# Optimization experiments

Hardware: AMD Instinct MI355X
Metric: run time of the kernel (lower is better)

Reference implementation:

```python
import jax, jax.numpy as jnp
import numpy as np

H = 64  # hidden size

def _uniform(key, shape, k):
    return jax.random.uniform(key, shape, jnp.float32, -k, k)

def setup_inputs() -> dict:
    key = jax.random.key(0)
    ks = jax.random.split(key, 20)
    k = 1.0 / np.sqrt(H)
    inp = {"x": jax.random.normal(ks[0], (4096, 512, 4), jnp.float32)}
    in_sizes = [4, H, H]
    for l in range(3):
        inp[f"w_ih{l}"] = _uniform(ks[1 + 4 * l], (H, in_sizes[l]), k)
        inp[f"w_hh{l}"] = _uniform(ks[2 + 4 * l], (H, H), k)
        inp[f"b_ih{l}"] = _uniform(ks[3 + 4 * l], (H,), k)
        inp[f"b_hh{l}"] = _uniform(ks[4 + 4 * l], (H,), k)
    inp["w1"] = _uniform(ks[13], (32, 64), 1.0 / np.sqrt(64))
    inp["bf1"] = _uniform(ks[14], (32,), 1.0 / np.sqrt(64))
    inp["w2"] = _uniform(ks[15], (16, 32), 1.0 / np.sqrt(32))
    inp["bf2"] = _uniform(ks[16], (16,), 1.0 / np.sqrt(32))
    inp["w3"] = _uniform(ks[17], (1, 16), 1.0 / np.sqrt(16))
    inp["bf3"] = _uniform(ks[18], (1,), 1.0 / np.sqrt(16))
    return inp


def _rnn_layer(x, w_ih, w_hh, b_ih, b_hh, last_only):
    # x: [B, T, I]; PyTorch RNN cell: h_t = tanh(x_t W_ih^T + b_ih + h_{t-1} W_hh^T + b_hh)
    xw = jnp.einsum('bti,hi->bth', x, w_ih) + (b_ih + b_hh)  # precompute input part
    h0 = jnp.zeros((x.shape[0], w_hh.shape[0]), x.dtype)

    def step(h, xt):
        h = jnp.tanh(xt + h @ w_hh.T)
        return h, (None if last_only else h)

    hT, ys = jax.lax.scan(step, h0, jnp.swapaxes(xw, 0, 1))  # scan over time
    if last_only:
        return hT  # [B, H]
    return jnp.swapaxes(ys, 0, 1)  # [B, T, H]


def reference(x, w_ih0, w_hh0, b_ih0, b_hh0, w_ih1, w_hh1, b_ih1, b_hh1,
              w_ih2, w_hh2, b_ih2, b_hh2, w1, bf1, w2, bf2, w3, bf3):
    h = _rnn_layer(x, w_ih0, w_hh0, b_ih0, b_hh0, last_only=False)
    h = _rnn_layer(h, w_ih1, w_hh1, b_ih1, b_hh1, last_only=False)
    h = _rnn_layer(h, w_ih2, w_hh2, b_ih2, b_hh2, last_only=True)  # only h[:, -1] is used
    h = jax.nn.relu(h @ w1.T + bf1)
    h = h @ w2.T + bf2
    return h @ w3.T + bf3  # [B, 1]
```

## Files before the change

kernel.cpp:

```cpp
#include <hip/hip_runtime.h>

typedef short s16;
typedef s16 bf16x8 __attribute__((ext_vector_type(8)));
typedef float f32x4 __attribute__((ext_vector_type(4)));
typedef unsigned int u32;
typedef unsigned short u16;

#define HST 72

__device__ __forceinline__ float fast_tanh(float x) {
    float e = __expf(2.0f * x);
    float r = __builtin_amdgcn_rcpf(e + 1.0f);
    return fmaf(-2.0f, r, 1.0f);
}

__device__ __forceinline__ u16 bfbits(float f) {
    u32 u = __builtin_bit_cast(u32, f);
    return (u16)((u + 0x7fffu + ((u >> 16) & 1u)) >> 16);
}

__device__ __forceinline__ void load_wfrag(const float* W, int i, int jb, bf16x8& hi, bf16x8& lo) {
    const float* p = W + i * 64 + jb;
#pragma unroll
    for (int e = 0; e < 8; ++e) {
        float f = p[e];
        u16 hb = bfbits(f);
        float fh = __builtin_bit_cast(float, ((u32)hb) << 16);
        hi[e] = (s16)hb;
        lo[e] = (s16)bfbits(f - fh);
    }
}

__device__ __forceinline__ void mm3(f32x4 acc[2], const bf16x8 wh[2], const bf16x8 wl[2],
                                    const bf16x8 bh[2], const bf16x8 bl[2]) {
#pragma unroll
    for (int c = 0; c < 2; ++c)
        acc[c] = __builtin_amdgcn_mfma_f32_16x16x32_bf16(wh[c], bh[c], acc[c], 0, 0, 0);
#pragma unroll
    for (int c = 0; c < 2; ++c)
        acc[c] = __builtin_amdgcn_mfma_f32_16x16x32_bf16(wh[c], bl[c], acc[c], 0, 0, 0);
#pragma unroll
    for (int c = 0; c < 2; ++c)
        acc[c] = __builtin_amdgcn_mfma_f32_16x16x32_bf16(wl[c], bh[c], acc[c], 0, 0, 0);
}

__device__ __forceinline__ void store_h(u16* hi_row, u16* lo_row, int nb, const float h[4]) {
    u16 hb[4], lb[4];
#pragma unroll
    for (int r = 0; r < 4; ++r) {
        hb[r] = bfbits(h[r]);
        float fh = __builtin_bit_cast(float, ((u32)hb[r]) << 16);
        lb[r] = bfbits(h[r] - fh);
    }
    uint2 hv, lv;
    hv.x = (u32)hb[0] | ((u32)hb[1] << 16);
    hv.y = (u32)hb[2] | ((u32)hb[3] << 16);
    lv.x = (u32)lb[0] | ((u32)lb[1] << 16);
    lv.y = (u32)lb[2] | ((u32)lb[3] << 16);
    *(uint2*)(hi_row + nb) = hv;
    *(uint2*)(lo_row + nb) = lv;
}

__device__ __forceinline__ void read_bfrag(const u16* hi_row, const u16* lo_row, int g,
                                           bf16x8 bh[2], bf16x8 bl[2]) {
#pragma unroll
    for (int c = 0; c < 2; ++c) {
        bh[c] = *(const bf16x8*)(hi_row + 32 * c + 8 * g);
        bl[c] = *(const bf16x8*)(lo_row + 32 * c + 8 * g);
    }
}

__global__ __launch_bounds__(256, 1)
void rnn3_fused(const float* __restrict__ x,
                const float* __restrict__ wih0, const float* __restrict__ whh0,
                const float* __restrict__ bih0, const float* __restrict__ bhh0,
                const float* __restrict__ wih1, const float* __restrict__ whh1,
                const float* __restrict__ bih1, const float* __restrict__ bhh1,
                const float* __restrict__ wih2, const float* __restrict__ whh2,
                const float* __restrict__ bih2, const float* __restrict__ bhh2,
                const float* __restrict__ w1, const float* __restrict__ bf1,
                const float* __restrict__ w2, const float* __restrict__ bf2,
                const float* __restrict__ w3, const float* __restrict__ bf3,
                float* __restrict__ out)
{
    __shared__ __align__(16) u16 Hhi[3][16][HST];
    __shared__ __align__(16) u16 Hlo[3][16][HST];
    __shared__ float hf[16][65];
    __shared__ float a1s[16][33];
    __shared__ float a2s[16][17];

    const int tid = (int)threadIdx.x;
    const int l = tid & 63;
    const int wv = tid >> 6;
    const int ml = l & 15;
    const int g = l >> 4;
    const int blk = (int)blockIdx.x;
    const int nb = wv * 16 + 4 * g;

    bf16x8 W0h[2], W0l[2], I1h[2], I1l[2], H1h[2], H1l[2], I2h[2], I2l[2], H2h[2], H2l[2];
    {
        int arow = wv * 16 + ml;
#pragma unroll
        for (int c = 0; c < 2; ++c) {
            int jb = 32 * c + 8 * g;
            load_wfrag(whh0, arow, jb, W0h[c], W0l[c]);
            load_wfrag(wih1, arow, jb, I1h[c], I1l[c]);
            load_wfrag(whh1, arow, jb, H1h[c], H1l[c]);
            load_wfrag(wih2, arow, jb, I2h[c], I2l[c]);
            load_wfrag(whh2, arow, jb, H2h[c], H2l[c]);
        }
    }
    float w0r[4][4], b0[4], b1[4], b2[4];
#pragma unroll
    for (int r = 0; r < 4; ++r) {
        int n = nb + r;
#pragma unroll
        for (int j = 0; j < 4; ++j) w0r[r][j] = wih0[n * 4 + j];
        b0[r] = bih0[n] + bhh0[n];
        b1[r] = bih1[n] + bhh1[n];
        b2[r] = bih2[n] + bhh2[n];
    }

    bf16x8 B0h[2], B0l[2], B1h[2], B1l[2], B2h[2], B2l[2];
#pragma unroll
    for (int c = 0; c < 2; ++c)
#pragma unroll
        for (int e = 0; e < 8; ++e) {
            B0h[c][e] = 0; B0l[c][e] = 0;
            B1h[c][e] = 0; B1l[c][e] = 0;
            B2h[c][e] = 0; B2l[c][e] = 0;
        }

    const float4* xv = (const float4*)x;
    const long xrow = (long)(blk * 16 + ml) * 512;
    float4 xn = xv[xrow];

    float h2v[4];

#pragma unroll 1
    for (int t = 0; t < 512; ++t) {
        float4 xc = xn;
        xn = xv[xrow + ((t + 1) & 511)];

        f32x4 a0[2], a1[2], a2[2];
        a0[0] = (f32x4){b0[0], b0[1], b0[2], b0[3]}; a0[1] = (f32x4){0.f, 0.f, 0.f, 0.f};
        a1[0] = (f32x4){b1[0], b1[1], b1[2], b1[3]}; a1[1] = (f32x4){0.f, 0.f, 0.f, 0.f};
        a2[0] = (f32x4){b2[0], b2[1], b2[2], b2[3]}; a2[1] = (f32x4){0.f, 0.f, 0.f, 0.f};
        mm3(a0, W0h, W0l, B0h, B0l);
        mm3(a1, H1h, H1l, B1h, B1l);
        mm3(a2, H2h, H2l, B2h, B2l);

        float hL[4];
#pragma unroll
        for (int r = 0; r < 4; ++r) {
            float s = a0[0][r] + a0[1][r];
            s = fmaf(xc.x, w0r[r][0], s);
            s = fmaf(xc.y, w0r[r][1], s);
            s = fmaf(xc.z, w0r[r][2], s);
            s = fmaf(xc.w, w0r[r][3], s);
            hL[r] = fast_tanh(s);
        }
        store_h(&Hhi[0][ml][0], &Hlo[0][ml][0], nb, hL);
        __syncthreads();
        read_bfrag(&Hhi[0][ml][0], &Hlo[0][ml][0], g, B0h, B0l);

        mm3(a1, I1h, I1l, B0h, B0l);
#pragma unroll
        for (int r = 0; r < 4; ++r) hL[r] = fast_tanh(a1[0][r] + a1[1][r]);
        store_h(&Hhi[1][ml][0], &Hlo[1][ml][0], nb, hL);
        __syncthreads();
        read_bfrag(&Hhi[1][ml][0], &Hlo[1][ml][0], g, B1h, B1l);

        mm3(a2, I2h, I2l, B1h, B1l);
#pragma unroll
        for (int r = 0; r < 4; ++r) { hL[r] = fast_tanh(a2[0][r] + a2[1][r]); h2v[r] = hL[r]; }
        store_h(&Hhi[2][ml][0], &Hlo[2][ml][0], nb, hL);
        __syncthreads();
        read_bfrag(&Hhi[2][ml][0], &Hlo[2][ml][0], g, B2h, B2l);
    }

#pragma unroll
    for (int r = 0; r < 4; ++r) hf[ml][nb + r] = h2v[r];
    __syncthreads();

    {
        int r = tid & 15, o2 = tid >> 4;
#pragma unroll
        for (int k = 0; k < 2; ++k) {
            int o = o2 * 2 + k;
            float s = bf1[o];
            for (int j = 0; j < 64; ++j) s = fmaf(hf[r][j], w1[o * 64 + j], s);
            a1s[r][o] = fmaxf(s, 0.f);
        }
    }
    __syncthreads();
    {
        int r = tid & 15, o = tid >> 4;
        float s = bf2[o];
        for (int j = 0; j < 32; ++j) s = fmaf(a1s[r][j], w2[o * 32 + j], s);
        a2s[r][o] = s;
    }
    __syncthreads();
    if (tid < 16) {
        float s = bf3[0];
        for (int j = 0; j < 16; ++j) s = fmaf(a2s[tid][j], w3[j], s);
        out[blk * 16 + tid] = s;
    }
}

extern "C" void kernel_launch(void* const* d_in, const int* in_sizes, int n_in,
                              void* d_out, int out_size, void* d_ws, size_t ws_size,
                              hipStream_t stream) {
    const float* x    = (const float*)d_in[0];
    const float* wih0 = (const float*)d_in[1];
    const float* whh0 = (const float*)d_in[2];
    const float* bih0 = (const float*)d_in[3];
    const float* bhh0 = (const float*)d_in[4];
    const float* wih1 = (const float*)d_in[5];
    const float* whh1 = (const float*)d_in[6];
    const float* bih1 = (const float*)d_in[7];
    const float* bhh1 = (const float*)d_in[8];
    const float* wih2 = (const float*)d_in[9];
    const float* whh2 = (const float*)d_in[10];
    const float* bih2 = (const float*)d_in[11];
    const float* bhh2 = (const float*)d_in[12];
    const float* w1   = (const float*)d_in[13];
    const float* bf1  = (const float*)d_in[14];
    const float* w2   = (const float*)d_in[15];
    const float* bf2  = (const float*)d_in[16];
    const float* w3   = (const float*)d_in[17];
    const float* bf3  = (const float*)d_in[18];

    rnn3_fused<<<dim3(256), dim3(256), 0, stream>>>(
        x, wih0, whh0, bih0, bhh0, wih1, whh1, bih1, bhh1,
        wih2, whh2, bih2, bhh2, w1, bf1, w2, bf2, w3, bf3,
        (float*)d_out);
}
```

Measured before the change: 578.3 us.

## Wavefront-pipeline the three RNN layers with one barrier per step

The three stacked layers are skewed in time, so layer 1 handles step p-1 and layer 2 handles step p-2 while layer 0 handles step p. All MFMA work in one iteration then becomes independent, and the three barriers per time step collapse to one. A double-buffered LDS hidden-state array, zero-initialised, removes write-after-read hazards. The cost is two extra prologue/epilogue iterations and predicated branches on the do flags.

New measurement: 696.8 us. +20.5%, slower.

```diff
diff --git a/kernel.cpp b/kernel.cpp
--- a/kernel.cpp
+++ b/kernel.cpp
@@ -83,8 +83,7 @@
                 const float* __restrict__ w3, const float* __restrict__ bf3,
                 float* __restrict__ out)
 {
-    __shared__ __align__(16) u16 Hhi[3][16][HST];
-    __shared__ __align__(16) u16 Hlo[3][16][HST];
+    __shared__ __align__(16) u16 H[2][2][3][16][HST];
     __shared__ float hf[16][65];
     __shared__ float a1s[16][33];
     __shared__ float a2s[16][17];
@@ -97,6 +96,12 @@
     const int blk = (int)blockIdx.x;
     const int nb = wv * 16 + 4 * g;
 
+    {
+        u32* hz = (u32*)&H[0][0][0][0][0];
+        const int nz = (int)(sizeof(H) / 4);
+        for (int i = tid; i < nz; i += 256) hz[i] = 0;
+    }
+
     bf16x8 W0h[2], W0l[2], I1h[2], I1l[2], H1h[2], H1l[2], I2h[2], I2l[2], H2h[2], H2l[2];
     {
         int arow = wv * 16 + ml;
@@ -135,48 +140,62 @@
     const long xrow = (long)(blk * 16 + ml) * 512;
     float4 xn = xv[xrow];
 
-    float h2v[4];
+    __syncthreads();
+
+    float h2v[4] = {0.f, 0.f, 0.f, 0.f};
 
 #pragma unroll 1
-    for (int t = 0; t < 512; ++t) {
+    for (int p = 0; p < 514; ++p) {
+        const int cur = p & 1;
         float4 xc = xn;
-        xn = xv[xrow + ((t + 1) & 511)];
+        xn = xv[xrow + ((p + 1) & 511)];
+
+        const bool do0 = (p < 512);
+        const bool do1 = (p >= 1) && (p <= 512);
+        const bool do2 = (p >= 2);
 
         f32x4 a0[2], a1[2], a2[2];
         a0[0] = (f32x4){b0[0], b0[1], b0[2], b0[3]}; a0[1] = (f32x4){0.f, 0.f, 0.f, 0.f};
         a1[0] = (f32x4){b1[0], b1[1], b1[2], b1[3]}; a1[1] = (f32x4){0.f, 0.f, 0.f, 0.f};
         a2[0] = (f32x4){b2[0], b2[1], b2[2], b2[3]}; a2[1] = (f32x4){0.f, 0.f, 0.f, 0.f};
-        mm3(a0, W0h, W0l, B0h, B0l);
-        mm3(a1, H1h, H1l, B1h, B1l);
-        mm3(a2, H2h, H2l, B2h, B2l);
-
-        float hL[4];
-#pragma unroll
-        for (int r = 0; r < 4; ++r) {
-            float s = a0[0][r] + a0[1][r];
-            s = fmaf(xc.x, w0r[r][0], s);
-            s = fmaf(xc.y, w0r[r][1], s);
-            s = fmaf(xc.z, w0r[r][2], s);
-            s = fmaf(xc.w, w0r[r][3], s);
-            hL[r] = fast_tanh(s);
-        }
-        store_h(&Hhi[0][ml][0], &Hlo[0][ml][0], nb, hL);
+
+        if (do0) mm3(a0, W0h, W0l, B0h, B0l);
+        if (do1) { mm3(a1, I1h, I1l, B0h, B0l);
+                   mm3(a1, H1h, H1l, B1h, B1l); }
+        if (do2) { mm3(a2, I2h, I2l, B1h, B1l);
+                   mm3(a2, H2h, H2l, B2h, B2l); }
+
+        if (do0) {
+            float hL[4];
+#pragma unroll
+            for (int r = 0; r < 4; ++r) {
+                float s = a0[0][r] + a0[1][r];
+                s = fmaf(xc.x, w0r[r][0], s);
+                s = fmaf(xc.y, w0r[r][1], s);
+                s = fmaf(xc.z, w0r[r][2], s);
+                s = fmaf(xc.w, w0r[r][3], s);
+                hL[r] = fast_tanh(s);
+            }
+            store_h(&H[cur][0][0][ml][0], &H[cur][1][0][ml][0], nb, hL);
+        }
+        if (do1) {
+            float hL[4];
+#pragma unroll
+            for (int r = 0; r < 4; ++r) hL[r] = fast_tanh(a1[0][r] + a1[1][r]);
+            store_h(&H[cur][0][1][ml][0], &H[cur][1][1][ml][0], nb, hL);
+        }
+        if (do2) {
+            float hL[4];
+#pragma unroll
+            for (int r = 0; r < 4; ++r) { hL[r] = fast_tanh(a2[0][r] + a2[1][r]); h2v[r] = hL[r]; }
+            store_h(&H[cur][0][2][ml][0], &H[cur][1][2][ml][0], nb, hL);
+        }
+
         __syncthreads();
-        read_bfrag(&Hhi[0][ml][0], &Hlo[0][ml][0], g, B0h, B0l);
-
-        mm3(a1, I1h, I1l, B0h, B0l);
-#pragma unroll
-        for (int r = 0; r < 4; ++r) hL[r] = fast_tanh(a1[0][r] + a1[1][r]);
-        store_h(&Hhi[1][ml][0], &Hlo[1][ml][0], nb, hL);
-        __syncthreads();
-        read_bfrag(&Hhi[1][ml][0], &Hlo[1][ml][0], g, B1h, B1l);
-
-        mm3(a2, I2h, I2l, B1h, B1l);
-#pragma unroll
-        for (int r = 0; r < 4; ++r) { hL[r] = fast_tanh(a2[0][r] + a2[1][r]); h2v[r] = hL[r]; }
-        store_h(&Hhi[2][ml][0], &Hlo[2][ml][0], nb, hL);
-        __syncthreads();
-        read_bfrag(&Hhi[2][ml][0], &Hlo[2][ml][0], g, B2h, B2l);
+
+        read_bfrag(&H[cur][0][0][ml][0], &H[cur][1][0][ml][0], g, B0h, B0l);
+        read_bfrag(&H[cur][0][1][ml][0], &H[cur][1][1][ml][0], g, B1h, B1l);
+        read_bfrag(&H[cur][0][2][ml][0], &H[cur][1][2][ml][0], g, B2h, B2l);
     }
 
 #pragma unroll
```
